# Kernel optimization log

Hardware: AMD Instinct MI355X
Metric: run time of the kernel (lower is better)

Reference implementation:

```python
import jax, jax.numpy as jnp
import numpy as np


def setup_inputs() -> dict:
    key = jax.random.key(0)
    kx, kd = jax.random.split(key)
    B, S, D = 32, 1024, 512
    x = jax.random.normal(kx, (B, S, D), dtype=jnp.float32)
    # per-token repeat counts in [1, 9): mean ~4.5 frames per phoneme
    durations = jax.random.randint(kd, (B, S), 1, 9, dtype=jnp.int32)
    return {"x": x, "durations": durations}


def reference(x, durations):
    """Duration-based token expansion (FastSpeech LengthRegulator).

    Replaces the per-token repeat/cat/pad Python loops with a single
    vectorized gather driven by cumulative duration offsets.
    Returns (expanded_x, mel_len, mel_mask) matching the torch module's
    (expanded_x, target=None, mel_len, mel_mask) with target omitted
    (projection is None in this configuration).
    """
    B, S, D = x.shape
    csum = jnp.cumsum(durations, axis=1)          # [B,S] end offset of each token
    mel_len = csum[:, -1]                         # [B]
    # max_len is data-dependent, same as the torch module's max over batch.
    max_len = int(jax.device_get(jnp.max(mel_len)))
    t = jnp.arange(max_len)                       # [T]
    # output frame t belongs to token j iff csum[j-1] <= t < csum[j]
    idx = jax.vmap(lambda c: jnp.searchsorted(c, t, side="right"))(csum)  # [B,T]
    idx = jnp.minimum(idx, S - 1)                 # clamp padding region
    expanded = jnp.take_along_axis(x, idx[:, :, None], axis=1)  # [B,T,D]
    mel_mask = t[None, :] >= mel_len[:, None]     # [B,T] True where padded
    expanded = jnp.where(mel_mask[:, :, None], jnp.zeros((), x.dtype), expanded)
    return expanded, mel_len, mel_mask
```

## Files before the change

kernel.cpp:

```cpp
#include <hip/hip_runtime.h>
#include <hip/hip_bf16.h>


#define S_TOK 1024
#define B_SZ  32
#define NBX   64

typedef float vfloat4 __attribute__((ext_vector_type(4)));

__global__ __launch_bounds__(64)
void lr_scan_kernel(const int* __restrict__ dur,
                    int* __restrict__ csum,
                    float* __restrict__ mel_len_out) {
    const int b = blockIdx.x;
    const int lane = threadIdx.x;
    const int* __restrict__ d = dur + b * S_TOK;

    int v[16];
    int sum = 0;
#pragma unroll
    for (int k = 0; k < 16; ++k) {
        v[k] = d[lane * 16 + k];
        sum += v[k];
    }
    int run = 0;
#pragma unroll
    for (int k = 0; k < 16; ++k) { run += v[k]; v[k] = run; }

    int tot = sum;
#pragma unroll
    for (int off = 1; off < 64; off <<= 1) {
        int n = __shfl_up(tot, off, 64);
        if (lane >= off) tot += n;
    }
    const int excl = tot - sum;

#pragma unroll
    for (int k = 0; k < 16; ++k)
        csum[b * S_TOK + lane * 16 + k] = v[k] + excl;
    if (lane == 63) mel_len_out[b] = (float)tot;
}

__global__ __launch_bounds__(256)
void lr_write_kernel(const float* __restrict__ x,
                     const int* __restrict__ csum,
                     float* __restrict__ out,
                     float* __restrict__ mask,
                     int D, int max_len) {
    const int b = blockIdx.y;
    const int tid = threadIdx.x;
    const int half = tid >> 7;
    const int lane = tid & 127;

    __shared__ __align__(16) int cs[S_TOK];
    ((int4*)cs)[tid] = ((const int4*)(csum + b * S_TOK))[tid];
    __syncthreads();
    const int mel = cs[S_TOK - 1];

    const int F = (max_len + NBX - 1) / NBX;
    const int t0 = blockIdx.x * F;
    const int tEnd = min(t0 + F, max_len);
    const int hF = (F + 1) >> 1;
    int t = min(t0 + half * hF, max_len);
    const int tend = min(t0 + (half ? F : hF), max_len);

    const float* __restrict__ xb = x + (size_t)b * S_TOK * (size_t)D;
    float* __restrict__ ob = out + (size_t)b * max_len * (size_t)D;

    const int dataEnd = min(tend, mel);

    if (t < dataEnd) {
        int lo = 0, hi = S_TOK;
        while (lo < hi) {
            int mid = (lo + hi) >> 1;
            if (cs[mid] > t) hi = mid; else lo = mid + 1;
        }
        int s = lo;
        vfloat4 v = ((const vfloat4*)(xb + (size_t)s * D))[lane];
        int cur = s;
        for (; t < dataEnd; ++t) {
            while (cs[s] <= t) ++s;
            if (s != cur) {
                v = ((const vfloat4*)(xb + (size_t)s * D))[lane];
                cur = s;
            }
            __builtin_nontemporal_store(v, (vfloat4*)(ob + (size_t)t * D) + lane);
        }
    }
    const vfloat4 z = (vfloat4)(0.f);
    for (; t < tend; ++t)
        __builtin_nontemporal_store(z, (vfloat4*)(ob + (size_t)t * D) + lane);

    float* __restrict__ mb = mask + (size_t)b * max_len;
    for (int u = t0 + tid; u < tEnd; u += 256)
        mb[u] = (u >= mel) ? 1.0f : 0.0f;
}

extern "C" void kernel_launch(void* const* d_in, const int* in_sizes, int n_in,
                              void* d_out, int out_size, void* d_ws, size_t ws_size,
                              hipStream_t stream) {
    const float* x = (const float*)d_in[0];
    const int* dur = (const int*)d_in[1];
    float* out = (float*)d_out;

    const int D = in_sizes[0] / in_sizes[1];
    const int max_len = (out_size / B_SZ - 1) / (D + 1);

    int* csum = (int*)d_ws;
    float* mel_len = out + (size_t)B_SZ * max_len * D;
    float* mask = mel_len + B_SZ;

    lr_scan_kernel<<<B_SZ, 64, 0, stream>>>(dur, csum, mel_len);

    dim3 grid(NBX, B_SZ);
    lr_write_kernel<<<grid, 256, 0, stream>>>(x, csum, out, mask, D, max_len);
}
```

Before: 363.1 us.

## Partition write kernel by source tokens and stage rows in shared memory

Each block now owns a contiguous group of 16 input tokens instead of a slice of output frames. It loads those 16 rows of x into shared memory with coalesced float4 loads and builds a small frame-to-token map, then streams the repeated rows out from LDS. This removes the per-block binary search and the serial scan over csum, and replaces repeated global reloads of x rows with one read per row. In exchange it uses 32KB of LDS per block, which may limit occupancy. Work per block now varies with the durations, and padding zeros are spread over blocks separately. D is hardcoded to 512.

```diff
diff --git a/kernel.cpp b/kernel.cpp
--- a/kernel.cpp
+++ b/kernel.cpp
@@ -4,7 +4,9 @@
 
 #define S_TOK 1024
 #define B_SZ  32
-#define NBX   64
+#define D_DIM 512
+#define TPB   16
+#define NBX   (S_TOK/TPB)
 
 typedef float vfloat4 __attribute__((ext_vector_type(4)));
 
@@ -46,54 +48,83 @@
                      const int* __restrict__ csum,
                      float* __restrict__ out,
                      float* __restrict__ mask,
-                     int D, int max_len) {
+                     int max_len) {
     const int b = blockIdx.y;
+    const int j = blockIdx.x;
     const int tid = threadIdx.x;
+    const int s0 = j * TPB;
+
+    __shared__ __align__(16) float rows[TPB * D_DIM];
+    __shared__ int cval[TPB + 1];
+    __shared__ unsigned char map[TPB * 8];
+    __shared__ int smel;
+
+    const int* __restrict__ cb = csum + b * S_TOK;
+    if (tid <= TPB) {
+        const int s = s0 - 1 + tid;
+        cval[tid] = (s < 0) ? 0 : cb[s];
+    }
+    if (tid == 255) smel = cb[S_TOK - 1];
+
+    {
+        const float4* __restrict__ src4 =
+            (const float4*)(x + ((size_t)b * S_TOK + s0) * D_DIM);
+        float4* __restrict__ dst4 = (float4*)rows;
+#pragma unroll
+        for (int k = 0; k < 8; ++k)
+            dst4[tid + k * 256] = src4[tid + k * 256];
+    }
+    __syncthreads();
+
+    const int fBase = cval[0];
+    const int fEnd = cval[TPB];
+    if (tid < TPB) {
+        const int lo = cval[tid], hi = cval[tid + 1];
+        for (int t = lo; t < hi; ++t) map[t - fBase] = (unsigned char)tid;
+    }
+    __syncthreads();
+
+    const int mel = smel;
     const int half = tid >> 7;
     const int lane = tid & 127;
+    float* __restrict__ ob = out + (size_t)b * max_len * D_DIM;
 
-    __shared__ __align__(16) int cs[S_TOK];
-    ((int4*)cs)[tid] = ((const int4*)(csum + b * S_TOK))[tid];
-    __syncthreads();
-    const int mel = cs[S_TOK - 1];
-
-    const int F = (max_len + NBX - 1) / NBX;
-    const int t0 = blockIdx.x * F;
-    const int tEnd = min(t0 + F, max_len);
-    const int hF = (F + 1) >> 1;
-    int t = min(t0 + half * hF, max_len);
-    const int tend = min(t0 + (half ? F : hF), max_len);
-
-    const float* __restrict__ xb = x + (size_t)b * S_TOK * (size_t)D;
-    float* __restrict__ ob = out + (size_t)b * max_len * (size_t)D;
-
-    const int dataEnd = min(tend, mel);
-
-    if (t < dataEnd) {
-        int lo = 0, hi = S_TOK;
-        while (lo < hi) {
-            int mid = (lo + hi) >> 1;
-            if (cs[mid] > t) hi = mid; else lo = mid + 1;
-        }
-        int s = lo;
-        vfloat4 v = ((const vfloat4*)(xb + (size_t)s * D))[lane];
-        int cur = s;
-        for (; t < dataEnd; ++t) {
-            while (cs[s] <= t) ++s;
-            if (s != cur) {
-                v = ((const vfloat4*)(xb + (size_t)s * D))[lane];
-                cur = s;
-            }
-            __builtin_nontemporal_store(v, (vfloat4*)(ob + (size_t)t * D) + lane);
+    {
+        const int span = fEnd - fBase;
+        const int hspan = (span + 1) >> 1;
+        int t = fBase + half * hspan;
+        const int tend = fBase + min(span, (half ? span : hspan));
+        for (; t < tend; ++t) {
+            const int r = map[t - fBase];
+            const vfloat4 v = ((const vfloat4*)(rows + r * D_DIM))[lane];
+            __builtin_nontemporal_store(v, (vfloat4*)(ob + (size_t)t * D_DIM) + lane);
         }
     }
-    const vfloat4 z = (vfloat4)(0.f);
-    for (; t < tend; ++t)
-        __builtin_nontemporal_store(z, (vfloat4*)(ob + (size_t)t * D) + lane);
 
-    float* __restrict__ mb = mask + (size_t)b * max_len;
-    for (int u = t0 + tid; u < tEnd; u += 256)
-        mb[u] = (u >= mel) ? 1.0f : 0.0f;
+    const int tail = max_len - mel;
+    if (tail > 0) {
+        const int chunk = (tail + NBX - 1) / NBX;
+        const int z0 = mel + j * chunk;
+        const int z1 = min(z0 + chunk, max_len);
+        if (z0 < z1) {
+            const int zn = z1 - z0;
+            const int hz = (zn + 1) >> 1;
+            int zt = z0 + half * hz;
+            const int zend = z0 + min(zn, (half ? zn : hz));
+            const vfloat4 zero = (vfloat4)(0.f);
+            for (; zt < zend; ++zt)
+                __builtin_nontemporal_store(zero, (vfloat4*)(ob + (size_t)zt * D_DIM) + lane);
+        }
+    }
+
+    {
+        const int seg = (max_len + NBX - 1) / NBX;
+        const int m0 = j * seg;
+        const int m1 = min(m0 + seg, max_len);
+        float* __restrict__ mb = mask + (size_t)b * max_len;
+        for (int u = m0 + tid; u < m1; u += 256)
+            mb[u] = (u >= mel) ? 1.0f : 0.0f;
+    }
 }
 
 extern "C" void kernel_launch(void* const* d_in, const int* in_sizes, int n_in,
@@ -113,5 +144,5 @@
     lr_scan_kernel<<<B_SZ, 64, 0, stream>>>(dur, csum, mel_len);
 
     dim3 grid(NBX, B_SZ);
-    lr_write_kernel<<<grid, 256, 0, stream>>>(x, csum, out, mask, D, max_len);
+    lr_write_kernel<<<grid, 256, 0, stream>>>(x, csum, out, mask, max_len);
 }
```

Result: no change. 359.7 us (-0.9%).
